# Kernel tuning notes

Measured on AMD Instinct MI355X. Metric: run time of the kernel, lower is better.

Reference implementation:

```python
import jax, jax.numpy as jnp
import numpy as np

D_K = 64
POS_WIN = 2.0

def setup_inputs() -> dict:
    key = jax.random.key(0)
    k1, k2, k3, k4 = jax.random.split(key, 4)
    B, H, S, D = 2, 8, 2048, D_K
    q = jax.random.normal(k1, (B, H, S, D), dtype=jnp.float32)
    k = jax.random.normal(k2, (B, H, S, D), dtype=jnp.float32)
    v = jax.random.normal(k3, (B, H, S, D), dtype=jnp.float32)
    # graph positional distances; module turns them into a Gaussian bias
    graph_attn_bias = jax.random.uniform(k4, (B, H, S, S), dtype=jnp.float32)
    return {"q": q, "k": k, "v": v, "graph_attn_bias": graph_attn_bias}

def reference(q, k, v, graph_attn_bias):
    # attn = (q / sqrt(d_k)) @ k^T  -> [B, H, Sq, Sk]
    scale = 1.0 / jnp.sqrt(jnp.float32(D_K))
    attn = jnp.einsum('bhqd,bhkd->bhqk', q * scale, k)
    # Gaussian positional bias: -0.5 * dist^2 / (0.5 * pos_win)^2
    gaussian_w = (-0.5 / (0.5 * POS_WIN) ** 2) * jnp.square(graph_attn_bias)
    attn = attn + gaussian_w
    weights = jax.nn.softmax(attn, axis=-1)  # dropout p=0.0 -> identity
    graph_out = jnp.einsum('bhqk,bhkd->bhqd', weights, v)
    return (graph_out, weights)
```

## Files before the change

kernel.cpp:

```cpp
#include <hip/hip_runtime.h>
#include <cstdint>

#define S 2048
#define D 64
#define QT 8
#define EPAD 8
#define ESTRIDE (S + EPAD)

typedef __attribute__((ext_vector_type(8))) short short8;
typedef __attribute__((ext_vector_type(4))) short short4v;
typedef __attribute__((ext_vector_type(4))) float floatx4;

static __device__ __forceinline__ unsigned short f2bf(float f) {
    union { float f; uint32_t u; } v; v.f = f;
    uint32_t r = (v.u + 0x7fffu + ((v.u >> 16) & 1u)) >> 16;
    return (unsigned short)r;
}
static __device__ __forceinline__ float bf2f(unsigned short s) {
    union { uint32_t u; float f; } v; v.u = ((uint32_t)s) << 16;
    return v.f;
}

__global__ void convert_bf16_kernel(const float* __restrict__ in,
                                    unsigned short* __restrict__ out, int n8) {
    int i = (blockIdx.x * 256 + threadIdx.x);
    if (i >= n8) return;
    const float* p = in + (size_t)i * 8;
    short8 o;
    #pragma unroll
    for (int j = 0; j < 8; ++j) o[j] = (short)f2bf(p[j]);
    *(short8*)(out + (size_t)i * 8) = o;
}

__global__ void transpose_v_kernel(const float* __restrict__ v,
                                   unsigned short* __restrict__ vt) {
    __shared__ unsigned short tile[64][72];
    const int tid = threadIdx.x;
    const int bh = blockIdx.x >> 5;
    const int s0 = (blockIdx.x & 31) * 64;
    #pragma unroll
    for (int rep = 0; rep < 16; ++rep) {
        int idx = rep * 256 + tid;
        int sl = idx >> 6, d = idx & 63;
        tile[sl][d] = f2bf(v[((size_t)bh * S + s0 + sl) * D + d]);
    }
    __syncthreads();
    #pragma unroll
    for (int rep = 0; rep < 16; ++rep) {
        int idx = rep * 256 + tid;
        int d = idx >> 6, sl = idx & 63;
        vt[((size_t)bh * D + d) * S + s0 + sl] = tile[sl][d];
    }
}

template <bool PRE>
__global__ __launch_bounds__(256, 4)
void attn_kernel(const float* __restrict__ q,
                 const float* __restrict__ k,
                 const float* __restrict__ v,
                 const float* __restrict__ bias,
                 const unsigned short* __restrict__ kb16,
                 const unsigned short* __restrict__ vt16,
                 float* __restrict__ gout,
                 float* __restrict__ wout)
{
    __shared__ __align__(16) unsigned short Elds[QT][ESTRIDE];
    __shared__ float rowsum[QT];

    const int tid  = threadIdx.x;
    const int wv   = tid >> 6;
    const int lane = tid & 63;
    const int quad = lane >> 4;
    const int l16  = lane & 15;

    const int bh = blockIdx.x >> 8;
    const int qt = blockIdx.x & 255;
    const int q0 = qt * QT;

    if (tid < QT) rowsum[tid] = 0.0f;
    __syncthreads();

    short8 aq[2];
    {
        const float* qrow = q + ((size_t)bh * S + q0 + (l16 & 7)) * D;
        #pragma unroll
        for (int s = 0; s < 2; ++s) {
            const float* p = qrow + s * 32 + quad * 8;
            #pragma unroll
            for (int j = 0; j < 8; ++j) aq[s][j] = (short)f2bf(p[j]);
        }
    }

    float psum[4] = {0.f, 0.f, 0.f, 0.f};
    for (int t = 0; t < 32; ++t) {
        const int kb = t * 64 + wv * 16;
        short8 bk[2];
        if (PRE) {
            const unsigned short* kr = kb16 + ((size_t)bh * S + kb + l16) * D;
            bk[0] = *(const short8*)(kr + quad * 8);
            bk[1] = *(const short8*)(kr + 32 + quad * 8);
        } else {
            const float* krow = k + ((size_t)bh * S + kb + l16) * D;
            #pragma unroll
            for (int s = 0; s < 2; ++s) {
                const float* p = krow + s * 32 + quad * 8;
                #pragma unroll
                for (int j = 0; j < 8; ++j) bk[s][j] = (short)f2bf(p[j]);
            }
        }
        floatx4 c = {0.f, 0.f, 0.f, 0.f};
        c = __builtin_amdgcn_mfma_f32_16x16x32_bf16(aq[0], bk[0], c, 0, 0, 0);
        c = __builtin_amdgcn_mfma_f32_16x16x32_bf16(aq[1], bk[1], c, 0, 0, 0);
        if (quad < 2) {
            #pragma unroll
            for (int r = 0; r < 4; ++r) {
                const int row = quad * 4 + r;
                const float b = bias[((size_t)bh * S + q0 + row) * S + kb + l16];
                const float logit = c[r] * 0.125f - 0.5f * b * b;
                const float e = __expf(logit);
                psum[r] += e;
                Elds[row][kb + l16] = f2bf(e);
            }
        }
    }
    if (quad < 2) {
        #pragma unroll
        for (int r = 0; r < 4; ++r) {
            float s0 = psum[r];
            s0 += __shfl_xor(s0, 1);
            s0 += __shfl_xor(s0, 2);
            s0 += __shfl_xor(s0, 4);
            s0 += __shfl_xor(s0, 8);
            if (l16 == 0) atomicAdd(&rowsum[quad * 4 + r], s0);
        }
    }

    __syncthreads();

    {
        const int r = tid >> 5;
        const int l = tid & 31;
        const float rinv = 1.0f / rowsum[r];
        float* wrow = wout + ((size_t)bh * S + q0 + r) * S;
        #pragma unroll 4
        for (int it = 0; it < 16; ++it) {
            const int col = it * 128 + l * 4;
            short4v ev = *(const short4v*)&Elds[r][col];
            floatx4 o;
            #pragma unroll
            for (int j = 0; j < 4; ++j) o[j] = bf2f((unsigned short)ev[j]) * rinv;
            *(floatx4*)(wrow + col) = o;
        }
    }

    {
        floatx4 acc = {0.f, 0.f, 0.f, 0.f};
        const int dimc = wv * 16 + l16;
        if (PRE) {
            const unsigned short* vrow = vt16 + ((size_t)bh * D + dimc) * S;
            for (int sl = 0; sl < 64; ++sl) {
                const int sbase = sl * 32;
                short8 af = *(const short8*)&Elds[l16 & 7][sbase + quad * 8];
                short8 bfv = *(const short8*)(vrow + sbase + quad * 8);
                acc = __builtin_amdgcn_mfma_f32_16x16x32_bf16(af, bfv, acc, 0, 0, 0);
            }
        } else {
            const float* vcol = v + (size_t)bh * S * D + dimc;
            for (int sl = 0; sl < 64; ++sl) {
                const int sbase = sl * 32;
                short8 af = *(const short8*)&Elds[l16 & 7][sbase + quad * 8];
                short8 bfv;
                #pragma unroll
                for (int j = 0; j < 8; ++j)
                    bfv[j] = (short)f2bf(vcol[(size_t)(sbase + quad * 8 + j) * D]);
                acc = __builtin_amdgcn_mfma_f32_16x16x32_bf16(af, bfv, acc, 0, 0, 0);
            }
        }
        if (quad < 2) {
            #pragma unroll
            for (int r = 0; r < 4; ++r) {
                const int row = quad * 4 + r;
                const float rinv = 1.0f / rowsum[row];
                gout[((size_t)bh * S + q0 + row) * D + dimc] = acc[r] * rinv;
            }
        }
    }
}

extern "C" void kernel_launch(void* const* d_in, const int* in_sizes, int n_in,
                              void* d_out, int out_size, void* d_ws, size_t ws_size,
                              hipStream_t stream) {
    const float* q    = (const float*)d_in[0];
    const float* k    = (const float*)d_in[1];
    const float* v    = (const float*)d_in[2];
    const float* bias = (const float*)d_in[3];
    const int BH = in_sizes[0] / (S * D);
    float* gout = (float*)d_out;
    float* wout = gout + (size_t)BH * S * D;

    const size_t nkv = (size_t)BH * S * D;
    const bool pre = ws_size >= nkv * 2 * sizeof(unsigned short);

    dim3 grid(BH * (S / QT));

    if (pre) {
        unsigned short* kb16 = (unsigned short*)d_ws;
        unsigned short* vt16 = kb16 + nkv;
        int n8 = (int)(nkv / 8);
        convert_bf16_kernel<<<(n8 + 255) / 256, 256, 0, stream>>>(k, kb16, n8);
        transpose_v_kernel<<<BH * (S / 64), 256, 0, stream>>>(v, vt16);
        attn_kernel<true><<<grid, dim3(256), 0, stream>>>(q, k, v, bias, kb16, vt16, gout, wout);
    } else {
        attn_kernel<false><<<grid, dim3(256), 0, stream>>>(q, k, v, bias, nullptr, nullptr, gout, wout);
    }
}
```

Before: 667.9 us.

## Double query tile, transpose QK MFMA operands, vectorize bias loads, split PV

Raises the query tile from 8 to 16 rows and the block from 256 to 512 threads. Swaps the MFMA operand roles so K is the A operand and Q is the B operand, which uses all 16 MFMA rows instead of discarding half. This lets each lane read four consecutive bias values as one float4 and write exp values to LDS as packed short4. The PV product is split across two key halves, reduced through a new shared pacc buffer with an extra barrier. LDS use per block roughly doubles, which reduces how many blocks fit on a CU.

Result: faster. 539.3 us (-19.3%).

```diff
diff --git a/kernel.cpp b/kernel.cpp
--- a/kernel.cpp
+++ b/kernel.cpp
@@ -3,7 +3,7 @@
 
 #define S 2048
 #define D 64
-#define QT 8
+#define QT 16
 #define EPAD 8
 #define ESTRIDE (S + EPAD)
 
@@ -54,7 +54,7 @@
 }
 
 template <bool PRE>
-__global__ __launch_bounds__(256, 4)
+__global__ __launch_bounds__(512, 4)
 void attn_kernel(const float* __restrict__ q,
                  const float* __restrict__ k,
                  const float* __restrict__ v,
@@ -65,6 +65,7 @@
                  float* __restrict__ wout)
 {
     __shared__ __align__(16) unsigned short Elds[QT][ESTRIDE];
+    __shared__ __align__(16) float pacc[QT][D];
     __shared__ float rowsum[QT];
 
     const int tid  = threadIdx.x;
@@ -73,67 +74,60 @@
     const int quad = lane >> 4;
     const int l16  = lane & 15;
 
-    const int bh = blockIdx.x >> 8;
-    const int qt = blockIdx.x & 255;
+    const int bh = blockIdx.x >> 7;
+    const int qt = blockIdx.x & 127;
     const int q0 = qt * QT;
 
     if (tid < QT) rowsum[tid] = 0.0f;
     __syncthreads();
 
-    short8 aq[2];
+    short8 bq[2];
     {
-        const float* qrow = q + ((size_t)bh * S + q0 + (l16 & 7)) * D;
+        const float* qrow = q + ((size_t)bh * S + q0 + l16) * D;
         #pragma unroll
         for (int s = 0; s < 2; ++s) {
             const float* p = qrow + s * 32 + quad * 8;
             #pragma unroll
-            for (int j = 0; j < 8; ++j) aq[s][j] = (short)f2bf(p[j]);
-        }
-    }
-
-    float psum[4] = {0.f, 0.f, 0.f, 0.f};
-    for (int t = 0; t < 32; ++t) {
-        const int kb = t * 64 + wv * 16;
-        short8 bk[2];
+            for (int j = 0; j < 8; ++j) bq[s][j] = (short)f2bf(p[j]);
+        }
+    }
+
+    const float* brow = bias + ((size_t)bh * S + q0 + l16) * S;
+
+    float psum = 0.0f;
+    for (int t = 0; t < 16; ++t) {
+        const int kb = t * 128 + wv * 16;
+        short8 ak[2];
         if (PRE) {
             const unsigned short* kr = kb16 + ((size_t)bh * S + kb + l16) * D;
-            bk[0] = *(const short8*)(kr + quad * 8);
-            bk[1] = *(const short8*)(kr + 32 + quad * 8);
+            ak[0] = *(const short8*)(kr + quad * 8);
+            ak[1] = *(const short8*)(kr + 32 + quad * 8);
         } else {
             const float* krow = k + ((size_t)bh * S + kb + l16) * D;
             #pragma unroll
             for (int s = 0; s < 2; ++s) {
                 const float* p = krow + s * 32 + quad * 8;
                 #pragma unroll
-                for (int j = 0; j < 8; ++j) bk[s][j] = (short)f2bf(p[j]);
+                for (int j = 0; j < 8; ++j) ak[s][j] = (short)f2bf(p[j]);
             }
         }
         floatx4 c = {0.f, 0.f, 0.f, 0.f};
-        c = __builtin_amdgcn_mfma_f32_16x16x32_bf16(aq[0], bk[0], c, 0, 0, 0);
-        c = __builtin_amdgcn_mfma_f32_16x16x32_bf16(aq[1], bk[1], c, 0, 0, 0);
-        if (quad < 2) {
-            #pragma unroll
-            for (int r = 0; r < 4; ++r) {
-                const int row = quad * 4 + r;
-                const float b = bias[((size_t)bh * S + q0 + row) * S + kb + l16];
-                const float logit = c[r] * 0.125f - 0.5f * b * b;
-                const float e = __expf(logit);
-                psum[r] += e;
-                Elds[row][kb + l16] = f2bf(e);
-            }
-        }
-    }
-    if (quad < 2) {
+        c = __builtin_amdgcn_mfma_f32_16x16x32_bf16(ak[0], bq[0], c, 0, 0, 0);
+        c = __builtin_amdgcn_mfma_f32_16x16x32_bf16(ak[1], bq[1], c, 0, 0, 0);
+        const floatx4 b4 = *(const floatx4*)(brow + kb + quad * 4);
+        short4v ev;
         #pragma unroll
         for (int r = 0; r < 4; ++r) {
-            float s0 = psum[r];
-            s0 += __shfl_xor(s0, 1);
-            s0 += __shfl_xor(s0, 2);
-            s0 += __shfl_xor(s0, 4);
-            s0 += __shfl_xor(s0, 8);
-            if (l16 == 0) atomicAdd(&rowsum[quad * 4 + r], s0);
-        }
-    }
+            const float logit = c[r] * 0.125f - 0.5f * b4[r] * b4[r];
+            const float e = __expf(logit);
+            psum += e;
+            ev[r] = (short)f2bf(e);
+        }
+        *(short4v*)&Elds[l16][kb + quad * 4] = ev;
+    }
+    psum += __shfl_xor(psum, 16);
+    psum += __shfl_xor(psum, 32);
+    if (lane < 16) atomicAdd(&rowsum[l16], psum);
 
     __syncthreads();
 
@@ -145,43 +139,52 @@
         #pragma unroll 4
         for (int it = 0; it < 16; ++it) {
             const int col = it * 128 + l * 4;
-            short4v ev = *(const short4v*)&Elds[r][col];
+            short4v evv = *(const short4v*)&Elds[r][col];
             floatx4 o;
             #pragma unroll
-            for (int j = 0; j < 4; ++j) o[j] = bf2f((unsigned short)ev[j]) * rinv;
+            for (int j = 0; j < 4; ++j) o[j] = bf2f((unsigned short)evv[j]) * rinv;
             *(floatx4*)(wrow + col) = o;
         }
     }
 
     {
+        const int dt = wv & 3;
+        const int kh = wv >> 2;
+        const int dimc = dt * 16 + l16;
         floatx4 acc = {0.f, 0.f, 0.f, 0.f};
-        const int dimc = wv * 16 + l16;
         if (PRE) {
-            const unsigned short* vrow = vt16 + ((size_t)bh * D + dimc) * S;
-            for (int sl = 0; sl < 64; ++sl) {
-                const int sbase = sl * 32;
-                short8 af = *(const short8*)&Elds[l16 & 7][sbase + quad * 8];
-                short8 bfv = *(const short8*)(vrow + sbase + quad * 8);
+            const unsigned short* vrow = vt16 + ((size_t)bh * D + dimc) * S + kh * 1024;
+            const unsigned short* erow = &Elds[l16][kh * 1024];
+            for (int sl = 0; sl < 32; ++sl) {
+                const int sb = sl * 32 + quad * 8;
+                short8 af  = *(const short8*)(erow + sb);
+                short8 bfv = *(const short8*)(vrow + sb);
                 acc = __builtin_amdgcn_mfma_f32_16x16x32_bf16(af, bfv, acc, 0, 0, 0);
             }
         } else {
             const float* vcol = v + (size_t)bh * S * D + dimc;
-            for (int sl = 0; sl < 64; ++sl) {
-                const int sbase = sl * 32;
-                short8 af = *(const short8*)&Elds[l16 & 7][sbase + quad * 8];
+            for (int sl = 0; sl < 32; ++sl) {
+                const int sb = kh * 1024 + sl * 32 + quad * 8;
+                short8 af = *(const short8*)&Elds[l16][sb];
                 short8 bfv;
                 #pragma unroll
                 for (int j = 0; j < 8; ++j)
-                    bfv[j] = (short)f2bf(vcol[(size_t)(sbase + quad * 8 + j) * D]);
+                    bfv[j] = (short)f2bf(vcol[(size_t)(sb + j) * D]);
                 acc = __builtin_amdgcn_mfma_f32_16x16x32_bf16(af, bfv, acc, 0, 0, 0);
             }
         }
-        if (quad < 2) {
+        if (kh == 1) {
+            #pragma unroll
+            for (int r = 0; r < 4; ++r) pacc[quad * 4 + r][dimc] = acc[r];
+        }
+        __syncthreads();
+        if (kh == 0) {
             #pragma unroll
             for (int r = 0; r < 4; ++r) {
                 const int row = quad * 4 + r;
                 const float rinv = 1.0f / rowsum[row];
-                gout[((size_t)bh * S + q0 + row) * D + dimc] = acc[r] * rinv;
+                gout[((size_t)bh * S + q0 + row) * D + dimc] =
+                    (acc[r] + pacc[row][dimc]) * rinv;
             }
         }
     }
@@ -209,8 +212,8 @@
         int n8 = (int)(nkv / 8);
         convert_bf16_kernel<<<(n8 + 255) / 256, 256, 0, stream>>>(k, kb16, n8);
         transpose_v_kernel<<<BH * (S / 64), 256, 0, stream>>>(v, vt16);
-        attn_kernel<true><<<grid, dim3(256), 0, stream>>>(q, k, v, bias, kb16, vt16, gout, wout);
+        attn_kernel<true><<<grid, dim3(512), 0, stream>>>(q, k, v, bias, kb16, vt16, gout, wout);
     } else {
-        attn_kernel<false><<<grid, dim3(256), 0, stream>>>(q, k, v, bias, nullptr, nullptr, gout, wout);
-    }
-}
+        attn_kernel<false><<<grid, dim3(512), 0, stream>>>(q, k, v, bias, nullptr, nullptr, gout, wout);
+    }
+}
```
